# Kernel optimization log

Hardware: AMD Instinct MI355X
Metric: run time of the kernel (lower is better)

The kernel has to match this reference:

```python
import jax, jax.numpy as jnp
import numpy as np

N_NODES = 100000
N_EDGES = 1600000
D_IN = 64
H = 64


def setup_inputs() -> dict:
    key = jax.random.key(0)
    ks = jax.random.split(key, 8)
    inp = {
        "x": jax.random.normal(ks[0], (N_NODES, D_IN), dtype=jnp.float32),
        "edge_index": jax.random.randint(ks[1], (2, N_EDGES), 0, N_NODES, dtype=jnp.int64),
        # layer 1 (SAGEConv): lin_l (aggregated neighbors, with bias), lin_r (root, no bias)
        "Wl1": jax.random.normal(ks[2], (D_IN, H), dtype=jnp.float32) / np.sqrt(D_IN),
        "bl1": jnp.zeros((H,), dtype=jnp.float32),
        "Wr1": jax.random.normal(ks[3], (D_IN, H), dtype=jnp.float32) / np.sqrt(D_IN),
        # layer 2
        "Wl2": jax.random.normal(ks[4], (H, H), dtype=jnp.float32) / np.sqrt(H),
        "bl2": jnp.zeros((H,), dtype=jnp.float32),
        "Wr2": jax.random.normal(ks[5], (H, H), dtype=jnp.float32) / np.sqrt(H),
        "Wfc": jax.random.normal(ks[6], (H, 1), dtype=jnp.float32) / np.sqrt(H),
        "bfc": jnp.zeros((1,), dtype=jnp.float32),
    }
    return inp


def _sage_conv(h, src, dst, inv_deg, Wl, bl, Wr):
    # mean-aggregate neighbor features: scatter-add messages then normalize by in-degree
    agg = jax.ops.segment_sum(h[src], dst, num_segments=N_NODES)  # [N, d]
    agg = agg * inv_deg[:, None]
    return agg @ Wl + bl + h @ Wr


def reference(x, edge_index, Wl1, bl1, Wr1, Wl2, bl2, Wr2, Wfc, bfc):
    src, dst = edge_index[0], edge_index[1]
    deg = jax.ops.segment_sum(jnp.ones((src.shape[0],), dtype=x.dtype), dst,
                              num_segments=N_NODES)
    inv_deg = jnp.where(deg > 0, 1.0 / jnp.maximum(deg, 1.0), 0.0)

    h = jax.nn.relu(_sage_conv(x, src, dst, inv_deg, Wl1, bl1, Wr1))
    h = jax.nn.relu(_sage_conv(h, src, dst, inv_deg, Wl2, bl2, Wr2))
    return h @ Wfc + bfc  # [N, 1]
```

## Files before the change

### kernel.cpp

```cpp
#include <hip/hip_runtime.h>
#include <hip/hip_fp16.h>

#define NN 100000
#define NE 1600000
#define SHIFT 7
#define NBUCK 782
#define P1B   782
#define EPB   2047

typedef _Float16 f16x8 __attribute__((ext_vector_type(8)));
typedef float f32x4 __attribute__((ext_vector_type(4)));
union H8U4 { f16x8 h; uint4 u; };

__device__ __forceinline__ int scan256(int* s, int t, int v) {
    s[t] = v;
    __syncthreads();
    for (int off = 1; off < 256; off <<= 1) {
        int add = (t >= off) ? s[t - off] : 0;
        __syncthreads();
        s[t] += add;
        __syncthreads();
    }
    return s[t];
}

__global__ __launch_bounds__(256) void k_hist(
    const float4* __restrict__ x4, ushort4* __restrict__ xh4,
    const float* __restrict__ Wl1, const float* __restrict__ Wr1, unsigned short* __restrict__ wt1,
    const float* __restrict__ Wl2, const float* __restrict__ Wr2, unsigned short* __restrict__ wt2,
    const int* __restrict__ dst, int* __restrict__ hist)
{
    __shared__ int h[NBUCK];
    int t = threadIdx.x, blk = blockIdx.x;

    const int n4 = NN * 16;
    const int per = (n4 + P1B - 1) / P1B;
    int cb = blk * per, ce = min(cb + per, n4);
    for (int i = cb + t; i < ce; i += 256) {
        float4 f = x4[i];
        _Float16 a = (_Float16)f.x, b = (_Float16)f.y, c = (_Float16)f.z, d = (_Float16)f.w;
        ushort4 u;
        u.x = *(unsigned short*)&a; u.y = *(unsigned short*)&b;
        u.z = *(unsigned short*)&c; u.w = *(unsigned short*)&d;
        xh4[i] = u;
    }
    if (blk < 64) {
        int idx = (blk & 31) * 256 + t;
        const float* Wl = (blk < 32) ? Wl1 : Wl2;
        const float* Wr = (blk < 32) ? Wr1 : Wr2;
        unsigned short* wt = (blk < 32) ? wt1 : wt2;
        int n = idx >> 7, k = idx & 127;
        float v = (k < 64) ? Wl[k * 64 + n] : Wr[(k - 64) * 64 + n];
        _Float16 hv = (_Float16)v;
        wt[idx] = *(unsigned short*)&hv;
    }

    for (int i = t; i < NBUCK; i += 256) h[i] = 0;
    __syncthreads();
    int eb = blk * EPB, ee = min(eb + EPB, NE);
    for (int e = eb + t; e < ee; e += 256) atomicAdd(&h[dst[e] >> SHIFT], 1);
    __syncthreads();
    for (int i = t; i < NBUCK; i += 256) hist[(size_t)i * P1B + blk] = h[i];
}

__global__ __launch_bounds__(256) void k_bin_total(const int* __restrict__ hist, int* __restrict__ bin_total) {
    __shared__ int sd[256];
    int b = blockIdx.x, t = threadIdx.x;
    int v = 0;
    for (int i = t; i < P1B; i += 256) v += hist[(size_t)b * P1B + i];
    sd[t] = v;
    __syncthreads();
    for (int s = 128; s > 0; s >>= 1) {
        if (t < s) sd[t] += sd[t + s];
        __syncthreads();
    }
    if (t == 0) bin_total[b] = sd[0];
}

__global__ __launch_bounds__(256) void k_cursor(int* __restrict__ hist, const int* __restrict__ bin_total,
                                                int* __restrict__ bucket_start, int* __restrict__ offsets) {
    __shared__ int sS[256];
    int b = blockIdx.x, t = threadIdx.x;

    int v = 0;
    for (int i = t; i < b; i += 256) v += bin_total[i];
    sS[t] = v;
    __syncthreads();
    for (int s = 128; s > 0; s >>= 1) {
        if (t < s) sS[t] += sS[t + s];
        __syncthreads();
    }
    int base = sS[0];
    __syncthreads();
    if (t == 0) bucket_start[b] = base;
    if (b == 0 && t == 0) { bucket_start[NBUCK] = NE; offsets[NN] = NE; }

    int carry = 0;
#pragma unroll
    for (int c = 0; c < 4; c++) {
        int idx = c * 256 + t;
        int hv = (idx < P1B) ? hist[(size_t)b * P1B + idx] : 0;
        int incl = scan256(sS, t, hv);
        if (idx < P1B) hist[(size_t)b * P1B + idx] = base + carry + incl - hv;
        __syncthreads();
        carry += sS[255];
        __syncthreads();
    }
}

__global__ __launch_bounds__(256) void k_scatter(const int* __restrict__ src, const int* __restrict__ dst,
                                                 const int* __restrict__ hist, unsigned int* __restrict__ pairs) {
    __shared__ int cur[NBUCK];
    int t = threadIdx.x, blk = blockIdx.x;
    for (int i = t; i < NBUCK; i += 256) cur[i] = hist[(size_t)i * P1B + blk];
    __syncthreads();
    int eb = blk * EPB, ee = min(eb + EPB, NE);
    for (int e = eb + t; e < ee; e += 256) {
        int d = dst[e];
        int pos = atomicAdd(&cur[d >> SHIFT], 1);
        pairs[pos] = (unsigned int)src[e] | ((unsigned int)(d & 127) << 17);
    }
}

__global__ __launch_bounds__(256) void k_bucket_csr(const unsigned int* __restrict__ pairs,
                                                    const int* __restrict__ bucket_start,
                                                    int* __restrict__ ssrc, int* __restrict__ offsets,
                                                    float* __restrict__ inv_deg) {
    __shared__ int cnt[128];
    __shared__ int sS[256];
    int b = blockIdx.x, t = threadIdx.x;
    if (t < 128) cnt[t] = 0;
    __syncthreads();
    int beg = bucket_start[b], end = bucket_start[b + 1];
    for (int e = beg + t; e < end; e += 256) atomicAdd(&cnt[pairs[e] >> 17], 1);
    __syncthreads();
    int deg = (t < 128) ? cnt[t] : 0;
    int incl = scan256(sS, t, deg);
    int ex = incl - deg;
    int node = (b << SHIFT) + t;
    if (t < 128 && node < NN) {
        offsets[node] = beg + ex;
        inv_deg[node] = (deg > 0) ? (1.0f / (float)deg) : 0.0f;
    }
    __syncthreads();
    if (t < 128) cnt[t] = beg + ex;
    __syncthreads();
    for (int e = beg + t; e < end; e += 256) {
        unsigned int pr = pairs[e];
        int pos = atomicAdd(&cnt[pr >> 17], 1);
        ssrc[pos] = (int)(pr & 0x1FFFFu);
    }
}

__global__ __launch_bounds__(256) void k_aggregate(const uint4* __restrict__ featq,
                                                   const int* __restrict__ ssrc,
                                                   const int* __restrict__ offsets, const float* __restrict__ inv_deg,
                                                   uint4* __restrict__ outq) {
    int node = blockIdx.x * 4 + (threadIdx.x >> 6);
    int lane = threadIdx.x & 63;
    if (node >= NN) return;
    int c = lane & 7, g = lane >> 3;
    int beg = offsets[node], end = offsets[node + 1];
    H8U4 acc;
    acc.h = (f16x8)(_Float16)0;
    int e = beg;

    for (; e + 16 <= end; e += 16) {
        int i0 = ssrc[e + g];
        int i1 = ssrc[e + 8 + g];
        H8U4 q0, q1;
        q0.u = featq[(size_t)i0 * 8 + c];
        q1.u = featq[(size_t)i1 * 8 + c];
        acc.h += q0.h;
        acc.h += q1.h;
    }
    for (; e < end; e += 8) {
        int m = end - e;
        int idx = ssrc[e + (g < m ? g : m - 1)];
        H8U4 q;
        q.u = featq[(size_t)idx * 8 + c];
        if (g < m) acc.h += q.h;
    }

#pragma unroll
    for (int mask = 8; mask <= 32; mask <<= 1) {
        H8U4 o;
        o.u.x = __shfl_xor(acc.u.x, mask);
        o.u.y = __shfl_xor(acc.u.y, mask);
        o.u.z = __shfl_xor(acc.u.z, mask);
        o.u.w = __shfl_xor(acc.u.w, mask);
        acc.h += o.h;
    }

    if (g == 0) {
        float s = inv_deg[node];
        H8U4 r;
#pragma unroll
        for (int j = 0; j < 8; j++) r.h[j] = (_Float16)((float)acc.h[j] * s);
        outq[(size_t)node * 8 + c] = r.u;
    }
}

template <bool FUSE_HEAD>
__global__ __launch_bounds__(256) void k_linear(const uint4* __restrict__ aggq, const uint4* __restrict__ rootq,
                                                const uint4* __restrict__ wtq,
                                                const float* __restrict__ bias,
                                                const float* __restrict__ Wfc, const float* __restrict__ bfc,
                                                float* __restrict__ out_f32, unsigned short* __restrict__ out_f16) {
    int tid = threadIdx.x;
    int wave = tid >> 6, lane = tid & 63;
    int nb = blockIdx.x * 64 + wave * 16;
    int m = lane & 15, quad = lane >> 4;

    int an = nb + m;
    if (an > NN - 1) an = NN - 1;
    H8U4 a[4];
    a[0].u = aggq[(size_t)an * 8 + quad];
    a[1].u = aggq[(size_t)an * 8 + 4 + quad];
    a[2].u = rootq[(size_t)an * 8 + quad];
    a[3].u = rootq[(size_t)an * 8 + 4 + quad];

    f32x4 acc[4];
#pragma unroll
    for (int n = 0; n < 4; n++) acc[n] = (f32x4){0.f, 0.f, 0.f, 0.f};

#pragma unroll
    for (int ncol = 0; ncol < 4; ncol++) {
        int col = ncol * 16 + m;
#pragma unroll
        for (int ki = 0; ki < 4; ki++) {
            H8U4 b;
            b.u = wtq[col * 16 + ki * 4 + quad];
            acc[ncol] = __builtin_amdgcn_mfma_f32_16x16x32_f16(a[ki].h, b.h, acc[ncol], 0, 0, 0);
        }
    }

    float bs[4];
#pragma unroll
    for (int ncol = 0; ncol < 4; ncol++) bs[ncol] = bias[ncol * 16 + m];

    if (!FUSE_HEAD) {
#pragma unroll
        for (int r = 0; r < 4; r++) {
            int node = nb + quad * 4 + r;
            if (node < NN) {
#pragma unroll
                for (int ncol = 0; ncol < 4; ncol++) {
                    float v = fmaxf(acc[ncol][r] + bs[ncol], 0.f);
                    _Float16 hv = (_Float16)v;
                    out_f16[(size_t)node * 64 + ncol * 16 + m] = *(unsigned short*)&hv;
                }
            }
        }
    } else {
        float wf[4];
#pragma unroll
        for (int ncol = 0; ncol < 4; ncol++) wf[ncol] = Wfc[ncol * 16 + m];
#pragma unroll
        for (int r = 0; r < 4; r++) {
            int node = nb + quad * 4 + r;
            float partial = 0.f;
#pragma unroll
            for (int ncol = 0; ncol < 4; ncol++)
                partial += fmaxf(acc[ncol][r] + bs[ncol], 0.f) * wf[ncol];
            partial += __shfl_xor(partial, 1);
            partial += __shfl_xor(partial, 2);
            partial += __shfl_xor(partial, 4);
            partial += __shfl_xor(partial, 8);
            if (m == 0 && node < NN) out_f32[node] = partial + bfc[0];
        }
    }
}

extern "C" void kernel_launch(void* const* d_in, const int* in_sizes, int n_in,
                              void* d_out, int out_size, void* d_ws, size_t ws_size,
                              hipStream_t stream) {
    const float* x   = (const float*)d_in[0];
    const int*   ei  = (const int*)d_in[1];
    const float* Wl1 = (const float*)d_in[2];
    const float* bl1 = (const float*)d_in[3];
    const float* Wr1 = (const float*)d_in[4];
    const float* Wl2 = (const float*)d_in[5];
    const float* bl2 = (const float*)d_in[6];
    const float* Wr2 = (const float*)d_in[7];
    const float* Wfc = (const float*)d_in[8];
    const float* bfc = (const float*)d_in[9];
    float* out = (float*)d_out;

    const int* srcp = ei;
    const int* dstp = ei + NE;

    char* p = (char*)d_ws;
    auto carve = [&](size_t bytes) {
        char* q = p;
        p += (bytes + 255) & ~size_t(255);
        return q;
    };
    int*            offsets = (int*)carve((size_t)(NN + 1) * 4);
    float*          inv_deg = (float*)carve((size_t)NN * 4);
    int*            ssrc    = (int*)carve((size_t)NE * 4);
    unsigned short* xh      = (unsigned short*)carve((size_t)NN * 64 * 2);
    unsigned short* h1h     = (unsigned short*)carve((size_t)NN * 64 * 2);
    unsigned short* aggh    = (unsigned short*)carve((size_t)NN * 64 * 2);
    unsigned short* wt1     = (unsigned short*)carve(64 * 128 * 2);
    unsigned short* wt2     = (unsigned short*)carve(64 * 128 * 2);
    unsigned int* pairs        = (unsigned int*)aggh;
    int*          hist         = (int*)(pairs + NE);
    int*          bin_total    = hist + (size_t)NBUCK * P1B;
    int*          bucket_start = bin_total + NBUCK;

    const int tile = (NN + 63) / 64;

    k_hist<<<P1B, 256, 0, stream>>>((const float4*)x, (ushort4*)xh,
                                    Wl1, Wr1, wt1, Wl2, Wr2, wt2, dstp, hist);
    k_bin_total<<<NBUCK, 256, 0, stream>>>(hist, bin_total);
    k_cursor<<<NBUCK, 256, 0, stream>>>(hist, bin_total, bucket_start, offsets);
    k_scatter<<<P1B, 256, 0, stream>>>(srcp, dstp, hist, pairs);
    k_bucket_csr<<<NBUCK, 256, 0, stream>>>(pairs, bucket_start, ssrc, offsets, inv_deg);

    k_aggregate<<<(NN + 3) / 4, 256, 0, stream>>>((const uint4*)xh, ssrc, offsets, inv_deg, (uint4*)aggh);
    k_linear<false><<<tile, 256, 0, stream>>>((const uint4*)aggh, (const uint4*)xh, (const uint4*)wt1,
                                              bl1, Wfc, bfc, nullptr, h1h);
    k_aggregate<<<(NN + 3) / 4, 256, 0, stream>>>((const uint4*)h1h, ssrc, offsets, inv_deg, (uint4*)aggh);
    k_linear<true><<<tile, 256, 0, stream>>>((const uint4*)aggh, (const uint4*)h1h, (const uint4*)wt2,
                                             bl2, Wfc, bfc, out, nullptr);
}
```

Before: 266.1 us.

## Double bucket size, fuse bin totals into histogram, aggregate two nodes per wave

Bucket width doubles from 128 to 256 nodes, halving the number of buckets and partition blocks, and the scan loop in k_cursor shrinks to two chunks. Per-bucket totals are now accumulated with global atomics inside k_hist after a memset, which removes the k_bin_total kernel launch. The aggregate kernel handles two destination nodes per wave with interleaved gathers, raising memory-level parallelism at the cost of more registers and imbalance when the two nodes have different degrees.

```diff
diff --git a/kernel.cpp b/kernel.cpp
--- a/kernel.cpp
+++ b/kernel.cpp
@@ -3,10 +3,10 @@
 
 #define NN 100000
 #define NE 1600000
-#define SHIFT 7
-#define NBUCK 782
-#define P1B   782
-#define EPB   2047
+#define SHIFT 8
+#define NBUCK 391
+#define P1B   391
+#define EPB   4093
 
 typedef _Float16 f16x8 __attribute__((ext_vector_type(8)));
 typedef float f32x4 __attribute__((ext_vector_type(4)));
@@ -28,7 +28,7 @@
     const float4* __restrict__ x4, ushort4* __restrict__ xh4,
     const float* __restrict__ Wl1, const float* __restrict__ Wr1, unsigned short* __restrict__ wt1,
     const float* __restrict__ Wl2, const float* __restrict__ Wr2, unsigned short* __restrict__ wt2,
-    const int* __restrict__ dst, int* __restrict__ hist)
+    const int* __restrict__ dst, int* __restrict__ hist, int* __restrict__ bin_total)
 {
     __shared__ int h[NBUCK];
     int t = threadIdx.x, blk = blockIdx.x;
@@ -60,21 +60,11 @@
     int eb = blk * EPB, ee = min(eb + EPB, NE);
     for (int e = eb + t; e < ee; e += 256) atomicAdd(&h[dst[e] >> SHIFT], 1);
     __syncthreads();
-    for (int i = t; i < NBUCK; i += 256) hist[(size_t)i * P1B + blk] = h[i];
-}
-
-__global__ __launch_bounds__(256) void k_bin_total(const int* __restrict__ hist, int* __restrict__ bin_total) {
-    __shared__ int sd[256];
-    int b = blockIdx.x, t = threadIdx.x;
-    int v = 0;
-    for (int i = t; i < P1B; i += 256) v += hist[(size_t)b * P1B + i];
-    sd[t] = v;
-    __syncthreads();
-    for (int s = 128; s > 0; s >>= 1) {
-        if (t < s) sd[t] += sd[t + s];
-        __syncthreads();
-    }
-    if (t == 0) bin_total[b] = sd[0];
+    for (int i = t; i < NBUCK; i += 256) {
+        int v = h[i];
+        hist[(size_t)i * P1B + blk] = v;
+        if (v) atomicAdd(&bin_total[i], v);
+    }
 }
 
 __global__ __launch_bounds__(256) void k_cursor(int* __restrict__ hist, const int* __restrict__ bin_total,
@@ -97,7 +87,7 @@
 
     int carry = 0;
 #pragma unroll
-    for (int c = 0; c < 4; c++) {
+    for (int c = 0; c < 2; c++) {
         int idx = c * 256 + t;
         int hv = (idx < P1B) ? hist[(size_t)b * P1B + idx] : 0;
         int incl = scan256(sS, t, hv);
@@ -118,7 +108,7 @@
     for (int e = eb + t; e < ee; e += 256) {
         int d = dst[e];
         int pos = atomicAdd(&cur[d >> SHIFT], 1);
-        pairs[pos] = (unsigned int)src[e] | ((unsigned int)(d & 127) << 17);
+        pairs[pos] = (unsigned int)src[e] | ((unsigned int)(d & 255) << 17);
     }
 }
 
@@ -126,24 +116,24 @@
                                                     const int* __restrict__ bucket_start,
                                                     int* __restrict__ ssrc, int* __restrict__ offsets,
                                                     float* __restrict__ inv_deg) {
-    __shared__ int cnt[128];
+    __shared__ int cnt[256];
     __shared__ int sS[256];
     int b = blockIdx.x, t = threadIdx.x;
-    if (t < 128) cnt[t] = 0;
+    cnt[t] = 0;
     __syncthreads();
     int beg = bucket_start[b], end = bucket_start[b + 1];
     for (int e = beg + t; e < end; e += 256) atomicAdd(&cnt[pairs[e] >> 17], 1);
     __syncthreads();
-    int deg = (t < 128) ? cnt[t] : 0;
+    int deg = cnt[t];
     int incl = scan256(sS, t, deg);
     int ex = incl - deg;
     int node = (b << SHIFT) + t;
-    if (t < 128 && node < NN) {
+    if (node < NN) {
         offsets[node] = beg + ex;
         inv_deg[node] = (deg > 0) ? (1.0f / (float)deg) : 0.0f;
     }
     __syncthreads();
-    if (t < 128) cnt[t] = beg + ex;
+    cnt[t] = beg + ex;
     __syncthreads();
     for (int e = beg + t; e < end; e += 256) {
         unsigned int pr = pairs[e];
@@ -156,48 +146,85 @@
                                                    const int* __restrict__ ssrc,
                                                    const int* __restrict__ offsets, const float* __restrict__ inv_deg,
                                                    uint4* __restrict__ outq) {
-    int node = blockIdx.x * 4 + (threadIdx.x >> 6);
+    int pairid = blockIdx.x * 4 + (threadIdx.x >> 6);
+    int node0 = pairid * 2;
+    if (node0 >= NN) return;
+    int node1 = node0 + 1;
+    bool has1 = node1 < NN;
     int lane = threadIdx.x & 63;
-    if (node >= NN) return;
     int c = lane & 7, g = lane >> 3;
-    int beg = offsets[node], end = offsets[node + 1];
-    H8U4 acc;
-    acc.h = (f16x8)(_Float16)0;
-    int e = beg;
-
-    for (; e + 16 <= end; e += 16) {
-        int i0 = ssrc[e + g];
-        int i1 = ssrc[e + 8 + g];
+
+    int beg0 = offsets[node0], end0 = offsets[node0 + 1];
+    int beg1 = has1 ? offsets[node1] : 0, end1 = has1 ? offsets[node1 + 1] : 0;
+    H8U4 acc0, acc1;
+    acc0.h = (f16x8)(_Float16)0;
+    acc1.h = (f16x8)(_Float16)0;
+    int e0 = beg0, e1 = beg1;
+
+    while (e0 + 16 <= end0 && e1 + 16 <= end1) {
+        int i00 = ssrc[e0 + g], i01 = ssrc[e0 + 8 + g];
+        int i10 = ssrc[e1 + g], i11 = ssrc[e1 + 8 + g];
+        H8U4 q00, q01, q10, q11;
+        q00.u = featq[(size_t)i00 * 8 + c];
+        q01.u = featq[(size_t)i01 * 8 + c];
+        q10.u = featq[(size_t)i10 * 8 + c];
+        q11.u = featq[(size_t)i11 * 8 + c];
+        acc0.h += q00.h; acc0.h += q01.h;
+        acc1.h += q10.h; acc1.h += q11.h;
+        e0 += 16; e1 += 16;
+    }
+    for (; e0 + 16 <= end0; e0 += 16) {
+        int i0 = ssrc[e0 + g], i1 = ssrc[e0 + 8 + g];
         H8U4 q0, q1;
         q0.u = featq[(size_t)i0 * 8 + c];
         q1.u = featq[(size_t)i1 * 8 + c];
-        acc.h += q0.h;
-        acc.h += q1.h;
-    }
-    for (; e < end; e += 8) {
-        int m = end - e;
-        int idx = ssrc[e + (g < m ? g : m - 1)];
+        acc0.h += q0.h; acc0.h += q1.h;
+    }
+    for (; e0 < end0; e0 += 8) {
+        int m = end0 - e0;
+        int idx = ssrc[e0 + (g < m ? g : m - 1)];
         H8U4 q;
         q.u = featq[(size_t)idx * 8 + c];
-        if (g < m) acc.h += q.h;
+        if (g < m) acc0.h += q.h;
+    }
+    for (; e1 + 16 <= end1; e1 += 16) {
+        int i0 = ssrc[e1 + g], i1 = ssrc[e1 + 8 + g];
+        H8U4 q0, q1;
+        q0.u = featq[(size_t)i0 * 8 + c];
+        q1.u = featq[(size_t)i1 * 8 + c];
+        acc1.h += q0.h; acc1.h += q1.h;
+    }
+    for (; e1 < end1; e1 += 8) {
+        int m = end1 - e1;
+        int idx = ssrc[e1 + (g < m ? g : m - 1)];
+        H8U4 q;
+        q.u = featq[(size_t)idx * 8 + c];
+        if (g < m) acc1.h += q.h;
     }
 
 #pragma unroll
     for (int mask = 8; mask <= 32; mask <<= 1) {
-        H8U4 o;
-        o.u.x = __shfl_xor(acc.u.x, mask);
-        o.u.y = __shfl_xor(acc.u.y, mask);
-        o.u.z = __shfl_xor(acc.u.z, mask);
-        o.u.w = __shfl_xor(acc.u.w, mask);
-        acc.h += o.h;
+        H8U4 o0, o1;
+        o0.u.x = __shfl_xor(acc0.u.x, mask); o0.u.y = __shfl_xor(acc0.u.y, mask);
+        o0.u.z = __shfl_xor(acc0.u.z, mask); o0.u.w = __shfl_xor(acc0.u.w, mask);
+        o1.u.x = __shfl_xor(acc1.u.x, mask); o1.u.y = __shfl_xor(acc1.u.y, mask);
+        o1.u.z = __shfl_xor(acc1.u.z, mask); o1.u.w = __shfl_xor(acc1.u.w, mask);
+        acc0.h += o0.h;
+        acc1.h += o1.h;
     }
 
     if (g == 0) {
-        float s = inv_deg[node];
+        float s0 = inv_deg[node0];
         H8U4 r;
 #pragma unroll
-        for (int j = 0; j < 8; j++) r.h[j] = (_Float16)((float)acc.h[j] * s);
-        outq[(size_t)node * 8 + c] = r.u;
+        for (int j = 0; j < 8; j++) r.h[j] = (_Float16)((float)acc0.h[j] * s0);
+        outq[(size_t)node0 * 8 + c] = r.u;
+        if (has1) {
+            float s1 = inv_deg[node1];
+#pragma unroll
+            for (int j = 0; j < 8; j++) r.h[j] = (_Float16)((float)acc1.h[j] * s1);
+            outq[(size_t)node1 * 8 + c] = r.u;
+        }
     }
 }
 
@@ -311,17 +338,18 @@
 
     const int tile = (NN + 63) / 64;
 
+    hipMemsetAsync(bin_total, 0, NBUCK * 4, stream);
     k_hist<<<P1B, 256, 0, stream>>>((const float4*)x, (ushort4*)xh,
-                                    Wl1, Wr1, wt1, Wl2, Wr2, wt2, dstp, hist);
-    k_bin_total<<<NBUCK, 256, 0, stream>>>(hist, bin_total);
+                                    Wl1, Wr1, wt1, Wl2, Wr2, wt2, dstp, hist, bin_total);
     k_cursor<<<NBUCK, 256, 0, stream>>>(hist, bin_total, bucket_start, offsets);
     k_scatter<<<P1B, 256, 0, stream>>>(srcp, dstp, hist, pairs);
     k_bucket_csr<<<NBUCK, 256, 0, stream>>>(pairs, bucket_start, ssrc, offsets, inv_deg);
 
-    k_aggregate<<<(NN + 3) / 4, 256, 0, stream>>>((const uint4*)xh, ssrc, offsets, inv_deg, (uint4*)aggh);
+    const int aggblocks = ((NN + 1) / 2 + 3) / 4;
+    k_aggregate<<<aggblocks, 256, 0, stream>>>((const uint4*)xh, ssrc, offsets, inv_deg, (uint4*)aggh);
     k_linear<false><<<tile, 256, 0, stream>>>((const uint4*)aggh, (const uint4*)xh, (const uint4*)wt1,
                                               bl1, Wfc, bfc, nullptr, h1h);
-    k_aggregate<<<(NN + 3) / 4, 256, 0, stream>>>((const uint4*)h1h, ssrc, offsets, inv_deg, (uint4*)aggh);
+    k_aggregate<<<aggblocks, 256, 0, stream>>>((const uint4*)h1h, ssrc, offsets, inv_deg, (uint4*)aggh);
     k_linear<true><<<tile, 256, 0, stream>>>((const uint4*)aggh, (const uint4*)h1h, (const uint4*)wt2,
                                              bl2, Wfc, bfc, out, nullptr);
 }
```

Measured after the change: 255.8 us (median of 2 runs). 3.9% less time.
